# Kernel tuning notes

Hardware: AMD Instinct MI355X
Metric: run time of the kernel (lower is better)

The kernel has to match this reference:

```python
import jax, jax.numpy as jnp
import numpy as np

INPUT_SIZE = 512
HIDDEN_SIZE = 512


def setup_inputs() -> dict:
    key = jax.random.key(0)
    k1, k2, k3, k4, k5 = jax.random.split(key, 5)
    B, N = 8, 2048
    x = jax.random.normal(k1, (B, N, INPUT_SIZE), dtype=jnp.float32)
    # Linear params (torch nn.Linear: y = x @ W^T + b), init scale ~ 1/sqrt(fan_in)
    s = 1.0 / np.sqrt(INPUT_SIZE)
    Wq = jax.random.uniform(k2, (HIDDEN_SIZE, INPUT_SIZE), minval=-s, maxval=s, dtype=jnp.float32)
    bq = jax.random.uniform(k3, (HIDDEN_SIZE,), minval=-s, maxval=s, dtype=jnp.float32)
    Wk = jax.random.uniform(k4, (HIDDEN_SIZE, INPUT_SIZE), minval=-s, maxval=s, dtype=jnp.float32)
    bk = jax.random.uniform(k5, (HIDDEN_SIZE,), minval=-s, maxval=s, dtype=jnp.float32)
    return {"x": x, "Wq": Wq, "bq": bq, "Wk": Wk, "bk": bk}


def reference(x, Wq, bq, Wk, bk):
    # q, k: [B, N, H]
    q = jnp.einsum('bnd,hd->bnh', x, Wq) + bq
    k = jnp.einsum('bnd,hd->bnh', x, Wk) + bk
    # scores: [B, N, N], softmax over last axis (dim=2)
    scores = jnp.einsum('bnh,bmh->bnm', q, k) / jnp.sqrt(jnp.float32(HIDDEN_SIZE))
    attn = jax.nn.softmax(scores, axis=2)
    # attended = attn^T @ x : [B, N, input_size]; squeeze(2) no-op since input_size>1
    attended = jnp.einsum('bnm,bnd->bmd', attn, x)
    return attended
```

## Files before the change

### kernel.cpp

```cpp
#include <hip/hip_runtime.h>

typedef __bf16 bf16x8 __attribute__((ext_vector_type(8)));
typedef __bf16 bf16x4 __attribute__((ext_vector_type(4)));
typedef float f32x4 __attribute__((ext_vector_type(4)));

__device__ __forceinline__ void async_copy16(const void* g, void* l) {
    __builtin_amdgcn_global_load_lds(
        (const __attribute__((address_space(1))) void*)g,
        (__attribute__((address_space(3))) void*)l, 16, 0, 0);
}

__device__ __forceinline__ int xcd_swz(int bx, int nx) {
    return (bx & 7) * (nx >> 3) + (bx >> 3);
}

__global__ __launch_bounds__(256) void k_cvt(
    const float4* __restrict__ x, const float4* __restrict__ Wq,
    const float4* __restrict__ Wk, const float4* __restrict__ bq,
    const float4* __restrict__ bk,
    bf16x4* __restrict__ xb, bf16x4* __restrict__ Wb,
    float4* __restrict__ biasc) {
    int i = blockIdx.x * 256 + threadIdx.x;
    if (i < 2097152) {
        float4 v = x[i];
        bf16x4 r = {(__bf16)v.x, (__bf16)v.y, (__bf16)v.z, (__bf16)v.w};
        xb[i] = r;
    }
    if (i < 131072) {
        float4 v = (i < 65536) ? Wq[i] : Wk[i - 65536];
        bf16x4 r = {(__bf16)v.x, (__bf16)v.y, (__bf16)v.z, (__bf16)v.w};
        Wb[i] = r;
    }
    if (i < 256) biasc[i] = (i < 128) ? bq[i] : bk[i - 128];
}

__global__ __launch_bounds__(256) void k_fold(
    const __bf16* __restrict__ xb, const float* __restrict__ Z,
    ushort* __restrict__ xzT) {
    __shared__ float tile[64][65];
    __shared__ float zin[64];
    const int b = blockIdx.y;
    const int td = blockIdx.x & 7;
    const int tn = blockIdx.x >> 3;
    const int n0 = tn * 64, d0 = td * 64;
    const int t = threadIdx.x;
    if (t < 64) zin[t] = 1.0f / Z[b * 2048 + n0 + t];
    __syncthreads();
    const int cl = t & 15, c4 = cl * 4, rr = t >> 4;
#pragma unroll
    for (int j = 0; j < 4; ++j) {
        int nr = rr + j * 16;
        bf16x4 v = *(const bf16x4*)&xb[((size_t)b * 2048 + n0 + nr) * 512 + d0 + c4];
        tile[nr][c4 + 0] = (float)v[0];
        tile[nr][c4 + 1] = (float)v[1];
        tile[nr][c4 + 2] = (float)v[2];
        tile[nr][c4 + 3] = (float)v[3];
    }
    __syncthreads();
#pragma unroll
    for (int j2 = 0; j2 < 4; ++j2) {
        int dr = rr + j2 * 16;
        bf16x4 pk;
#pragma unroll
        for (int j = 0; j < 4; ++j)
            pk[j] = (__bf16)(tile[j * 16 + cl][dr] * zin[c4 + j]);
        *(bf16x4*)&xzT[((size_t)b * 512 + d0 + dr) * 2048 + n0 + c4] = pk;
    }
}

template <int EPI>
__device__ __forceinline__ void gemm8p(
    const ushort* __restrict__ A, int lda, long sA,
    const ushort* __restrict__ B, int ldb, long sB,
    ushort* __restrict__ C, int ldc, long sC,
    int tiles_n, int K,
    const float* __restrict__ bias, float scale2,
    float* __restrict__ Z, long sZ) {
    extern __shared__ char lds[];
    const int b = blockIdx.y;
    A += (size_t)b * sA;
    B += (size_t)b * sB;
    const int bx = xcd_swz(blockIdx.x, gridDim.x);
    const int tm = bx / tiles_n, tn = bx % tiles_n;
    const int t = threadIdx.x;
    const int l = t & 63, w = t >> 6;
    const int wr = w >> 2, wc = w & 3;
    const int l15 = l & 15, g16 = l >> 4;

    size_t gAo[2], gBo[2];
    int dst[2];
#pragma unroll
    for (int p = 0; p < 2; ++p) {
        int off = p * 8192 + t * 16;
        int P = off >> 7, sl = (off >> 4) & 7;
        int u = sl ^ (P & 7);
        int rg = 2 * P + (u >> 2);
        int kb8 = (u & 3) * 8;
        gAo[p] = (size_t)(tm * 256 + rg) * lda + kb8;
        gBo[p] = (size_t)(tn * 256 + rg) * ldb + kb8;
        dst[p] = off;
    }

#define REG_A(d, ks) (((d) * 2 + (ks)) * 16384)
#define REG_B(d, ks) (65536 + ((d) * 2 + (ks)) * 16384)
#define STG_A(d, ks, kk)                                              \
    { int ro = REG_A(d, ks);                                          \
      async_copy16(A + gAo[0] + (kk), lds + ro + dst[0]);             \
      async_copy16(A + gAo[1] + (kk), lds + ro + dst[1]); }
#define STG_B(d, ks, kk)                                              \
    { int ro = REG_B(d, ks);                                          \
      async_copy16(B + gBo[0] + (kk), lds + ro + dst[0]);             \
      async_copy16(B + gBo[1] + (kk), lds + ro + dst[1]); }

    auto rdoff = [&](int row) {
        int P = row >> 1;
        int slot = (((row & 1) << 2) | g16) ^ (P & 7);
        return P * 128 + slot * 16;
    };

    f32x4 acc[8][4];
#pragma unroll
    for (int i = 0; i < 8; ++i)
#pragma unroll
        for (int j = 0; j < 4; ++j) acc[i][j] = (f32x4){0.f, 0.f, 0.f, 0.f};

    bf16x8 af[4], bg[4];

#define RD_B(d, ks)                                                   \
    _Pragma("unroll") for (int j = 0; j < 4; ++j)                     \
        bg[j] = *(const bf16x8*)(lds + REG_B(d, ks) +                 \
                                 rdoff(wc * 64 + j * 16 + l15));
#define RD_A(d, ks, isub)                                             \
    _Pragma("unroll") for (int i = 0; i < 4; ++i)                     \
        af[i] = *(const bf16x8*)(lds + REG_A(d, ks) +                 \
                                 rdoff(wr * 128 + (isub) * 64 + i * 16 + l15));
#define DO_MFMA(isub)                                                 \
    __builtin_amdgcn_s_setprio(1);                                    \
    _Pragma("unroll") for (int i = 0; i < 4; ++i)                     \
        _Pragma("unroll") for (int j = 0; j < 4; ++j)                 \
            acc[(isub) * 4 + i][j] = __builtin_amdgcn_mfma_f32_16x16x32_bf16( \
                af[i], bg[j], acc[(isub) * 4 + i][j], 0, 0, 0);       \
    __builtin_amdgcn_s_setprio(0);
#define SYNC_LGKM                                                     \
    asm volatile("s_waitcnt lgkmcnt(0)" ::: "memory");                \
    __builtin_amdgcn_sched_barrier(0);
#define ENDPH(vm)                                                     \
    if (vm) asm volatile("s_waitcnt vmcnt(4)" ::: "memory");          \
    __builtin_amdgcn_s_barrier();                                     \
    asm volatile("" ::: "memory");                                    \
    __builtin_amdgcn_sched_barrier(0);

    STG_B(0, 0, 0); STG_A(0, 0, 0);
    STG_B(0, 1, 32); STG_A(0, 1, 32);
    STG_B(1, 0, 64); STG_A(1, 0, 64);
    asm volatile("s_waitcnt vmcnt(4)" ::: "memory");
    __builtin_amdgcn_s_barrier();
    asm volatile("" ::: "memory");

    const int NI = K >> 7;
    for (int it = 0; it < NI; ++it) {
        const int kb = it << 7;
        const int kn = (it + 1 < NI) ? (kb + 128) : kb;
        RD_B(0, 0); RD_A(0, 0, 0); STG_B(1, 1, kb + 96);
        SYNC_LGKM; DO_MFMA(0); ENDPH(false);
        RD_A(0, 0, 1); STG_A(1, 1, kb + 96);
        SYNC_LGKM; DO_MFMA(1); ENDPH(false);
        RD_B(0, 1); RD_A(0, 1, 0); STG_B(0, 0, kn);
        SYNC_LGKM; DO_MFMA(0); ENDPH(false);
        RD_A(0, 1, 1); STG_A(0, 0, kn);
        SYNC_LGKM; DO_MFMA(1); ENDPH(true);
        RD_B(1, 0); RD_A(1, 0, 0); STG_B(0, 1, kn + 32);
        SYNC_LGKM; DO_MFMA(0); ENDPH(false);
        RD_A(1, 0, 1); STG_A(0, 1, kn + 32);
        SYNC_LGKM; DO_MFMA(1); ENDPH(false);
        RD_B(1, 1); RD_A(1, 1, 0); STG_B(1, 0, kn + 64);
        SYNC_LGKM; DO_MFMA(0); ENDPH(false);
        RD_A(1, 1, 1); STG_A(1, 0, kn + 64);
        SYNC_LGKM; DO_MFMA(1); ENDPH(true);
    }
    asm volatile("s_waitcnt vmcnt(0)" ::: "memory");

    const int mb = tm * 256 + wr * 128;
    const int nb = tn * 256 + wc * 64;
    const int cl = l15;
    ushort* Cp = C + (size_t)b * sC;

    if (EPI == 0) {
#pragma unroll
        for (int i = 0; i < 8; ++i)
#pragma unroll
            for (int q = 0; q < 4; ++q) {
                int row = mb + i * 16 + (l >> 4) * 4 + q;
                bf16x4 pk;
#pragma unroll
                for (int j = 0; j < 4; ++j)
                    pk[j] = (__bf16)(acc[i][j][q] + bias[nb + j * 16 + cl]);
                *(bf16x4*)&Cp[(size_t)row * ldc + nb + cl * 4] = pk;
            }
    } else {
        float colsum[4] = {0.f, 0.f, 0.f, 0.f};
#pragma unroll
        for (int i = 0; i < 8; ++i)
#pragma unroll
            for (int q = 0; q < 4; ++q) {
                int row = mb + i * 16 + (l >> 4) * 4 + q;
                bf16x4 pk;
#pragma unroll
                for (int j = 0; j < 4; ++j) {
                    float e = __builtin_amdgcn_exp2f(acc[i][j][q] * scale2);
                    colsum[j] += e;
                    pk[j] = (__bf16)e;
                }
                *(bf16x4*)&Cp[(size_t)row * ldc + nb + cl * 4] = pk;
            }
#pragma unroll
        for (int j = 0; j < 4; ++j) {
            float s = colsum[j];
            s += __shfl_xor(s, 16);
            s += __shfl_xor(s, 32);
            if (l < 16) atomicAdd(&Z[b * sZ + nb + l * 4 + j], s);
        }
    }
#undef REG_A
#undef REG_B
#undef STG_A
#undef STG_B
#undef RD_A
#undef RD_B
#undef DO_MFMA
#undef SYNC_LGKM
#undef ENDPH
}

__global__ __launch_bounds__(512, 2) void k_proj8(
    const ushort* __restrict__ A, const ushort* __restrict__ B,
    ushort* __restrict__ C, const float* __restrict__ bias) {
    gemm8p<0>(A, 512, 0L, B, 512, 0L, C, 1024, 0L,
              4, 512, bias, 0.f, nullptr, 0L);
}

__global__ __launch_bounds__(512, 2) void k_escore8(
    const ushort* __restrict__ A, const ushort* __restrict__ B,
    ushort* __restrict__ C, float* __restrict__ Z) {
    gemm8p<1>(A, 1024, 2048L * 1024, B, 1024, 2048L * 1024,
              C, 2048, 2048L * 2048, 8, 512,
              nullptr, 0.063758716f, Z, 2048L);
}

__global__ __launch_bounds__(256) void k_out(
    const ushort* __restrict__ Ain, const ushort* __restrict__ Bin,
    float* __restrict__ Cout) {
    __shared__ ushort lA[2][8192];
    __shared__ ushort lB[2][8192];
    const int lda = 2048, ldb = 2048, ldc = 512, tiles_n = 4, K = 2048;
    const int b = blockIdx.y;
    const ushort* A = Ain + (size_t)b * 2048L * 2048;
    const ushort* B = Bin + (size_t)b * 512L * 2048;
    const int bx = xcd_swz(blockIdx.x, gridDim.x);
    const int tm = bx / tiles_n, tn = bx % tiles_n;
    const int t = threadIdx.x;
    const int l = t & 63, w = t >> 6;
    const int wr = w >> 1, wc = w & 1;

    size_t gA[4], gB[4];
    int dOf[4];
#pragma unroll
    for (int p = 0; p < 4; ++p) {
        int off = p * 4096 + t * 16;
        int row = off >> 7, kb = off & 127;
        int kswz = kb ^ ((row & 7) << 4);
        gA[p] = (size_t)(tm * 128 + row) * lda + (kswz >> 1);
        gB[p] = (size_t)(tn * 128 + row) * ldb + (kswz >> 1);
        dOf[p] = off;
    }
    auto stage = [&](int buf, int k0) {
#pragma unroll
        for (int p = 0; p < 4; ++p) {
            async_copy16(A + gA[p] + k0, (char*)lA[buf] + dOf[p]);
            async_copy16(B + gB[p] + k0, (char*)lB[buf] + dOf[p]);
        }
    };

    f32x4 acc[4][4];
#pragma unroll
    for (int i = 0; i < 4; ++i)
#pragma unroll
        for (int j = 0; j < 4; ++j) acc[i][j] = (f32x4){0.f, 0.f, 0.f, 0.f};

    const int nk = K >> 6;
    stage(0, 0);
    stage(1, 64);
    asm volatile("s_waitcnt vmcnt(8)" ::: "memory");
    __builtin_amdgcn_s_barrier();
    asm volatile("" ::: "memory");

    for (int kt = 0; kt < nk; ++kt) {
        const int cur = kt & 1;
        bf16x8 af[4][2], bg[4][2];
#pragma unroll
        for (int ks = 0; ks < 2; ++ks)
#pragma unroll
            for (int i = 0; i < 4; ++i) {
                int rowA = wr * 64 + i * 16 + (l & 15);
                int colA = (ks * 64 + (l >> 4) * 16) ^ ((rowA & 7) << 4);
                af[i][ks] = *(const bf16x8*)((const char*)lA[cur] + rowA * 128 + colA);
                int rowB = wc * 64 + i * 16 + (l & 15);
                int colB = (ks * 64 + (l >> 4) * 16) ^ ((rowB & 7) << 4);
                bg[i][ks] = *(const bf16x8*)((const char*)lB[cur] + rowB * 128 + colB);
            }
        asm volatile("s_waitcnt lgkmcnt(0)" ::: "memory");
        __builtin_amdgcn_sched_barrier(0);
        __builtin_amdgcn_s_barrier();
        asm volatile("" ::: "memory");
        if (kt + 2 < nk) stage(cur, (kt + 2) << 6);
        __builtin_amdgcn_sched_barrier(0);
        __builtin_amdgcn_s_setprio(1);
#pragma unroll
        for (int ks = 0; ks < 2; ++ks)
#pragma unroll
            for (int i = 0; i < 4; ++i)
#pragma unroll
                for (int j = 0; j < 4; ++j)
                    acc[i][j] = __builtin_amdgcn_mfma_f32_16x16x32_bf16(
                        af[i][ks], bg[j][ks], acc[i][j], 0, 0, 0);
        __builtin_amdgcn_s_setprio(0);
        if (kt + 2 < nk) {
            asm volatile("s_waitcnt vmcnt(8)" ::: "memory");
        } else {
            asm volatile("s_waitcnt vmcnt(0)" ::: "memory");
        }
        __builtin_amdgcn_s_barrier();
        asm volatile("" ::: "memory");
    }

    const int mb = tm * 128 + wr * 64;
    const int nb = tn * 128 + wc * 64;
    float* Cp = Cout + (size_t)b * 2048L * 512;
#pragma unroll
    for (int i = 0; i < 4; ++i)
#pragma unroll
        for (int j = 0; j < 4; ++j)
#pragma unroll
            for (int q = 0; q < 4; ++q) {
                int row = mb + i * 16 + (l >> 4) * 4 + q;
                int col = nb + j * 16 + (l & 15);
                Cp[(size_t)row * ldc + col] = acc[i][j][q];
            }
}

namespace {
struct AttrInit {
    AttrInit() {
        hipFuncSetAttribute(reinterpret_cast<const void*>(&k_proj8),
                            hipFuncAttributeMaxDynamicSharedMemorySize, 131072);
        hipFuncSetAttribute(reinterpret_cast<const void*>(&k_escore8),
                            hipFuncAttributeMaxDynamicSharedMemorySize, 131072);
    }
};
AttrInit attr_init_;
}

extern "C" void kernel_launch(void* const* d_in, const int* in_sizes, int n_in,
                              void* d_out, int out_size, void* d_ws, size_t ws_size,
                              hipStream_t stream) {
    const float* x  = (const float*)d_in[0];
    const float* Wq = (const float*)d_in[1];
    const float* bq = (const float*)d_in[2];
    const float* Wk = (const float*)d_in[3];
    const float* bk = (const float*)d_in[4];

    char* ws = (char*)d_ws;
    ushort* xb    = (ushort*)(ws);
    ushort* Wb    = (ushort*)(ws + 16777216);
    float*  biasc = (float*) (ws + 17825792);
    float*  Z     = (float*) (ws + 17829888);
    ushort* qkb   = (ushort*)(ws + 17895424);
    ushort* E     = (ushort*)(ws + 51449856);
    ushort* xzT   = qkb;

    (void)hipMemsetAsync(Z, 0, 16384 * 4, stream);

    k_cvt<<<8192, 256, 0, stream>>>(
        (const float4*)x, (const float4*)Wq, (const float4*)Wk,
        (const float4*)bq, (const float4*)bk,
        (bf16x4*)xb, (bf16x4*)Wb, (float4*)biasc);

    k_proj8<<<dim3(256, 1), 512, 131072, stream>>>(xb, Wb, qkb, biasc);

    k_escore8<<<dim3(64, 8), 512, 131072, stream>>>(qkb + 512, qkb, E, Z);

    k_fold<<<dim3(256, 8), 256, 0, stream>>>((const __bf16*)xb, Z, xzT);

    k_out<<<dim3(64, 8), 256, 0, stream>>>(E, xzT, (float*)d_out);
}
```

Baseline: 127.5 us.

## Fuse x fp32-to-bf16 conversion into the QK projection GEMM

The separate full-tensor conversion of x to bf16 is removed. The projection GEMM now loads fp32 x directly, converts it in registers, writes it to LDS, and has the tn==0 blocks also write the bf16 copy of x that the later fold kernel reads. The weight conversion kernel now also zeroes Z, which replaces the memset. The projection moves from a 256x256 tile with 512 threads to a new 128x128 tile kernel with 256 threads and register-staged A loads. The goal is to cut one read-write pass over x and a launch, at the cost of a less tuned projection GEMM that reads fp32 x once per N-tile.

```diff
diff --git a/kernel.cpp b/kernel.cpp
--- a/kernel.cpp
+++ b/kernel.cpp
@@ -14,24 +14,17 @@
     return (bx & 7) * (nx >> 3) + (bx >> 3);
 }
 
-__global__ __launch_bounds__(256) void k_cvt(
-    const float4* __restrict__ x, const float4* __restrict__ Wq,
-    const float4* __restrict__ Wk, const float4* __restrict__ bq,
-    const float4* __restrict__ bk,
-    bf16x4* __restrict__ xb, bf16x4* __restrict__ Wb,
-    float4* __restrict__ biasc) {
+__global__ __launch_bounds__(256) void k_cvtw(
+    const float4* __restrict__ Wq, const float4* __restrict__ Wk,
+    const float4* __restrict__ bq, const float4* __restrict__ bk,
+    bf16x4* __restrict__ Wb, float4* __restrict__ biasc,
+    float4* __restrict__ Z) {
     int i = blockIdx.x * 256 + threadIdx.x;
-    if (i < 2097152) {
-        float4 v = x[i];
-        bf16x4 r = {(__bf16)v.x, (__bf16)v.y, (__bf16)v.z, (__bf16)v.w};
-        xb[i] = r;
-    }
-    if (i < 131072) {
-        float4 v = (i < 65536) ? Wq[i] : Wk[i - 65536];
-        bf16x4 r = {(__bf16)v.x, (__bf16)v.y, (__bf16)v.z, (__bf16)v.w};
-        Wb[i] = r;
-    }
+    float4 v = (i < 65536) ? Wq[i] : Wk[i - 65536];
+    bf16x4 r = {(__bf16)v.x, (__bf16)v.y, (__bf16)v.z, (__bf16)v.w};
+    Wb[i] = r;
     if (i < 256) biasc[i] = (i < 128) ? bq[i] : bk[i - 128];
+    if (i < 4096) Z[i] = (float4){0.f, 0.f, 0.f, 0.f};
 }
 
 __global__ __launch_bounds__(256) void k_fold(
@@ -68,18 +61,147 @@
     }
 }
 
-template <int EPI>
-__device__ __forceinline__ void gemm8p(
-    const ushort* __restrict__ A, int lda, long sA,
-    const ushort* __restrict__ B, int ldb, long sB,
-    ushort* __restrict__ C, int ldc, long sC,
-    int tiles_n, int K,
-    const float* __restrict__ bias, float scale2,
-    float* __restrict__ Z, long sZ) {
+__global__ __launch_bounds__(256) void k_projf(
+    const float* __restrict__ X, const ushort* __restrict__ Wb,
+    ushort* __restrict__ qkb, ushort* __restrict__ xb,
+    const float* __restrict__ bias) {
+    __shared__ ushort lA[2][8192];
+    __shared__ ushort lB[2][8192];
+    const int ldc = 1024, tiles_n = 8, K = 512;
+    const int bx = xcd_swz(blockIdx.x, gridDim.x);
+    const int tm = bx / tiles_n, tn = bx % tiles_n;
+    const int t = threadIdx.x;
+    const int l = t & 63, w = t >> 6;
+    const int wr = w >> 1, wc = w & 1;
+
+    const int ar = t >> 1, ah = t & 1;
+    const float* xrow = X + (size_t)(tm * 128 + ar) * 512 + ah * 32;
+    ushort* xbrow = xb + (size_t)(tm * 128 + ar) * 512 + ah * 32;
+    int wOf[4];
+#pragma unroll
+    for (int w4 = 0; w4 < 4; ++w4)
+        wOf[w4] = ar * 128 + (((ah * 4 + w4) * 16) ^ ((ar & 7) << 4));
+
+    size_t gB[4];
+    int dOf[4];
+#pragma unroll
+    for (int p = 0; p < 4; ++p) {
+        int off = p * 4096 + t * 16;
+        int row = off >> 7, kb = off & 127;
+        int kswz = kb ^ ((row & 7) << 4);
+        gB[p] = (size_t)(tn * 128 + row) * 512 + (kswz >> 1);
+        dOf[p] = off;
+    }
+    auto stageB = [&](int buf, int k0) {
+#pragma unroll
+        for (int p = 0; p < 4; ++p)
+            async_copy16(Wb + gB[p] + k0, (char*)lB[buf] + dOf[p]);
+    };
+
+    float4 rA[8];
+    auto loadA = [&](int k0) {
+#pragma unroll
+        for (int c = 0; c < 8; ++c)
+            rA[c] = *(const float4*)(xrow + k0 + c * 4);
+    };
+    auto cvtwrite = [&](int buf, int k0) {
+#pragma unroll
+        for (int w4 = 0; w4 < 4; ++w4) {
+            float4 a = rA[2 * w4], b2 = rA[2 * w4 + 1];
+            bf16x8 v8 = {(__bf16)a.x, (__bf16)a.y, (__bf16)a.z, (__bf16)a.w,
+                         (__bf16)b2.x, (__bf16)b2.y, (__bf16)b2.z, (__bf16)b2.w};
+            *(bf16x8*)((char*)lA[buf] + wOf[w4]) = v8;
+            if (tn == 0) *(bf16x8*)(xbrow + k0 + w4 * 8) = v8;
+        }
+    };
+
+    f32x4 acc[4][4];
+#pragma unroll
+    for (int i = 0; i < 4; ++i)
+#pragma unroll
+        for (int j = 0; j < 4; ++j) acc[i][j] = (f32x4){0.f, 0.f, 0.f, 0.f};
+
+    const int nk = K >> 6;
+    stageB(0, 0);
+    loadA(0);
+    asm volatile("s_waitcnt vmcnt(0)" ::: "memory");
+    cvtwrite(0, 0);
+    stageB(1, 64);
+    asm volatile("s_waitcnt lgkmcnt(0)" ::: "memory");
+    __builtin_amdgcn_s_barrier();
+    asm volatile("" ::: "memory");
+
+    for (int kt = 0; kt < nk; ++kt) {
+        const int cur = kt & 1, nxt = cur ^ 1;
+        bf16x8 af[4][2], bg[4][2];
+#pragma unroll
+        for (int ks = 0; ks < 2; ++ks)
+#pragma unroll
+            for (int i = 0; i < 4; ++i) {
+                int rowA = wr * 64 + i * 16 + (l & 15);
+                int colA = (ks * 64 + (l >> 4) * 16) ^ ((rowA & 7) << 4);
+                af[i][ks] = *(const bf16x8*)((const char*)lA[cur] + rowA * 128 + colA);
+                int rowB = wc * 64 + i * 16 + (l & 15);
+                int colB = (ks * 64 + (l >> 4) * 16) ^ ((rowB & 7) << 4);
+                bg[i][ks] = *(const bf16x8*)((const char*)lB[cur] + rowB * 128 + colB);
+            }
+        if (kt + 1 < nk) loadA((kt + 1) << 6);
+        asm volatile("s_waitcnt lgkmcnt(0)" ::: "memory");
+        __builtin_amdgcn_sched_barrier(0);
+        __builtin_amdgcn_s_barrier();
+        asm volatile("" ::: "memory");
+        if (kt + 2 < nk) stageB(cur, (kt + 2) << 6);
+        __builtin_amdgcn_sched_barrier(0);
+        __builtin_amdgcn_s_setprio(1);
+#pragma unroll
+        for (int ks = 0; ks < 2; ++ks)
+#pragma unroll
+            for (int i = 0; i < 4; ++i)
+#pragma unroll
+                for (int j = 0; j < 4; ++j)
+                    acc[i][j] = __builtin_amdgcn_mfma_f32_16x16x32_bf16(
+                        af[i][ks], bg[j][ks], acc[i][j], 0, 0, 0);
+        __builtin_amdgcn_s_setprio(0);
+        if (kt + 1 < nk) {
+            if (kt + 2 < nk) {
+                asm volatile("s_waitcnt vmcnt(4)" ::: "memory");
+            } else {
+                asm volatile("s_waitcnt vmcnt(0)" ::: "memory");
+            }
+            __builtin_amdgcn_sched_barrier(0);
+            cvtwrite(nxt, (kt + 1) << 6);
+            asm volatile("s_waitcnt lgkmcnt(0)" ::: "memory");
+        }
+        __builtin_amdgcn_s_barrier();
+        asm volatile("" ::: "memory");
+    }
+
+    const int mb = tm * 128 + wr * 64;
+    const int nb = tn * 128 + wc * 64;
+    const int cl = l & 15;
+#pragma unroll
+    for (int i = 0; i < 4; ++i)
+#pragma unroll
+        for (int q = 0; q < 4; ++q) {
+            int row = mb + i * 16 + (l >> 4) * 4 + q;
+            bf16x4 pk;
+#pragma unroll
+            for (int j = 0; j < 4; ++j)
+                pk[j] = (__bf16)(acc[i][j][q] + bias[nb + j * 16 + cl]);
+            *(bf16x4*)&qkb[(size_t)row * ldc + nb + cl * 4] = pk;
+        }
+}
+
+__global__ __launch_bounds__(512, 2) void k_escore8(
+    const ushort* __restrict__ Ain, const ushort* __restrict__ Bin,
+    ushort* __restrict__ Cout, float* __restrict__ Z) {
     extern __shared__ char lds[];
+    const int lda = 1024, ldb = 1024, ldc = 2048, tiles_n = 8, K = 512;
+    const long sA = 2048L * 1024, sB = 2048L * 1024, sC = 2048L * 2048, sZ = 2048;
+    const float scale2 = 0.063758716f;
     const int b = blockIdx.y;
-    A += (size_t)b * sA;
-    B += (size_t)b * sB;
+    const ushort* A = Ain + (size_t)b * sA;
+    const ushort* B = Bin + (size_t)b * sB;
     const int bx = xcd_swz(blockIdx.x, gridDim.x);
     const int tm = bx / tiles_n, tn = bx % tiles_n;
     const int t = threadIdx.x;
@@ -183,43 +305,28 @@
     const int mb = tm * 256 + wr * 128;
     const int nb = tn * 256 + wc * 64;
     const int cl = l15;
-    ushort* Cp = C + (size_t)b * sC;
-
-    if (EPI == 0) {
-#pragma unroll
-        for (int i = 0; i < 8; ++i)
-#pragma unroll
-            for (int q = 0; q < 4; ++q) {
-                int row = mb + i * 16 + (l >> 4) * 4 + q;
-                bf16x4 pk;
-#pragma unroll
-                for (int j = 0; j < 4; ++j)
-                    pk[j] = (__bf16)(acc[i][j][q] + bias[nb + j * 16 + cl]);
-                *(bf16x4*)&Cp[(size_t)row * ldc + nb + cl * 4] = pk;
+    ushort* Cp = Cout + (size_t)b * sC;
+    float colsum[4] = {0.f, 0.f, 0.f, 0.f};
+#pragma unroll
+    for (int i = 0; i < 8; ++i)
+#pragma unroll
+        for (int q = 0; q < 4; ++q) {
+            int row = mb + i * 16 + (l >> 4) * 4 + q;
+            bf16x4 pk;
+#pragma unroll
+            for (int j = 0; j < 4; ++j) {
+                float e = __builtin_amdgcn_exp2f(acc[i][j][q] * scale2);
+                colsum[j] += e;
+                pk[j] = (__bf16)e;
             }
-    } else {
-        float colsum[4] = {0.f, 0.f, 0.f, 0.f};
-#pragma unroll
-        for (int i = 0; i < 8; ++i)
-#pragma unroll
-            for (int q = 0; q < 4; ++q) {
-                int row = mb + i * 16 + (l >> 4) * 4 + q;
-                bf16x4 pk;
-#pragma unroll
-                for (int j = 0; j < 4; ++j) {
-                    float e = __builtin_amdgcn_exp2f(acc[i][j][q] * scale2);
-                    colsum[j] += e;
-                    pk[j] = (__bf16)e;
-                }
-                *(bf16x4*)&Cp[(size_t)row * ldc + nb + cl * 4] = pk;
-            }
-#pragma unroll
-        for (int j = 0; j < 4; ++j) {
-            float s = colsum[j];
-            s += __shfl_xor(s, 16);
-            s += __shfl_xor(s, 32);
-            if (l < 16) atomicAdd(&Z[b * sZ + nb + l * 4 + j], s);
-        }
+            *(bf16x4*)&Cp[(size_t)row * ldc + nb + cl * 4] = pk;
+        }
+#pragma unroll
+    for (int j = 0; j < 4; ++j) {
+        float s = colsum[j];
+        s += __shfl_xor(s, 16);
+        s += __shfl_xor(s, 32);
+        if (l < 16) atomicAdd(&Z[b * sZ + nb + l * 4 + j], s);
     }
 #undef REG_A
 #undef REG_B
@@ -230,21 +337,6 @@
 #undef DO_MFMA
 #undef SYNC_LGKM
 #undef ENDPH
-}
-
-__global__ __launch_bounds__(512, 2) void k_proj8(
-    const ushort* __restrict__ A, const ushort* __restrict__ B,
-    ushort* __restrict__ C, const float* __restrict__ bias) {
-    gemm8p<0>(A, 512, 0L, B, 512, 0L, C, 1024, 0L,
-              4, 512, bias, 0.f, nullptr, 0L);
-}
-
-__global__ __launch_bounds__(512, 2) void k_escore8(
-    const ushort* __restrict__ A, const ushort* __restrict__ B,
-    ushort* __restrict__ C, float* __restrict__ Z) {
-    gemm8p<1>(A, 1024, 2048L * 1024, B, 1024, 2048L * 1024,
-              C, 2048, 2048L * 2048, 8, 512,
-              nullptr, 0.063758716f, Z, 2048L);
 }
 
 __global__ __launch_bounds__(256) void k_out(
@@ -351,8 +443,6 @@
 namespace {
 struct AttrInit {
     AttrInit() {
-        hipFuncSetAttribute(reinterpret_cast<const void*>(&k_proj8),
-                            hipFuncAttributeMaxDynamicSharedMemorySize, 131072);
         hipFuncSetAttribute(reinterpret_cast<const void*>(&k_escore8),
                             hipFuncAttributeMaxDynamicSharedMemorySize, 131072);
     }
@@ -378,14 +468,13 @@
     ushort* E     = (ushort*)(ws + 51449856);
     ushort* xzT   = qkb;
 
-    (void)hipMemsetAsync(Z, 0, 16384 * 4, stream);
-
-    k_cvt<<<8192, 256, 0, stream>>>(
-        (const float4*)x, (const float4*)Wq, (const float4*)Wk,
+    k_cvtw<<<512, 256, 0, stream>>>(
+        (const float4*)Wq, (const float4*)Wk,
         (const float4*)bq, (const float4*)bk,
-        (bf16x4*)xb, (bf16x4*)Wb, (float4*)biasc);
-
-    k_proj8<<<dim3(256, 1), 512, 131072, stream>>>(xb, Wb, qkb, biasc);
+        (bf16x4*)Wb, (float4*)biasc, (float4*)Z);
+
+    k_projf<<<dim3(1024, 1), 256, 0, stream>>>(
+        x, Wb, qkb, xb, biasc);
 
     k_escore8<<<dim3(64, 8), 512, 131072, stream>>>(qkb + 512, qkb, E, Z);
 
```

New measurement: 168.8 us. 1.32x slower.
